# Optimization experiments

Measured on AMD Instinct MI355X. Metric: run time of the kernel, lower is better.

## Reference

```python
import jax, jax.numpy as jnp
import numpy as np

DIM = 64          # out_channels == mamba d_model
D_INNER = 2 * DIM # mamba expand=2
D_STATE = 16
DT_RANK = 4       # ceil(DIM/16)
D_CONV = 4


def setup_inputs() -> dict:
    key = jax.random.key(0)
    ks = jax.random.split(key, 12)
    B, Cin, H, W = 4, 32, 192, 192
    x = jax.random.normal(ks[0], (B, Cin, H, W), jnp.float32)
    conv_w = jax.random.normal(ks[1], (DIM, Cin, 4, 4), jnp.float32) * (1.0 / np.sqrt(Cin * 16))
    conv_b = jnp.zeros((DIM,), jnp.float32)
    ln_g = jnp.ones((DIM,), jnp.float32)
    ln_b = jnp.zeros((DIM,), jnp.float32)
    in_proj_w = jax.random.normal(ks[2], (2 * D_INNER, DIM), jnp.float32) * (1.0 / np.sqrt(DIM))
    conv1d_w = jax.random.normal(ks[3], (D_INNER, 1, D_CONV), jnp.float32) * (1.0 / np.sqrt(D_CONV))
    conv1d_b = jnp.zeros((D_INNER,), jnp.float32)
    x_proj_w = jax.random.normal(ks[4], (DT_RANK + 2 * D_STATE, D_INNER), jnp.float32) * (1.0 / np.sqrt(D_INNER))
    dt_proj_w = jax.random.normal(ks[5], (D_INNER, DT_RANK), jnp.float32) * (DT_RANK ** -0.5)
    dt_proj_b = jnp.log(jnp.expm1(jnp.exp(jax.random.uniform(ks[6], (D_INNER,), jnp.float32,
                jnp.log(1e-3), jnp.log(1e-1)))))  # softplus-inverse of dt in [1e-3,1e-1]
    A_log = jnp.log(jnp.tile(jnp.arange(1, D_STATE + 1, dtype=jnp.float32)[None, :], (D_INNER, 1)))
    D = jnp.ones((D_INNER,), jnp.float32)
    out_proj_w = jax.random.normal(ks[7], (DIM, D_INNER), jnp.float32) * (1.0 / np.sqrt(D_INNER))
    return {"x": x, "conv_w": conv_w, "conv_b": conv_b, "ln_g": ln_g, "ln_b": ln_b,
            "in_proj_w": in_proj_w, "conv1d_w": conv1d_w, "conv1d_b": conv1d_b,
            "x_proj_w": x_proj_w, "dt_proj_w": dt_proj_w, "dt_proj_b": dt_proj_b,
            "A_log": A_log, "D": D, "out_proj_w": out_proj_w}


def _mamba(seq, in_proj_w, conv1d_w, conv1d_b, x_proj_w, dt_proj_w, dt_proj_b, A_log, D, out_proj_w):
    # seq: (B, L, DIM)
    Bb, L, _ = seq.shape
    xz = seq @ in_proj_w.T                          # (B, L, 2*d_inner)
    xm, z = jnp.split(xz, 2, axis=-1)
    # causal depthwise conv1d along L
    xc = jnp.transpose(xm, (0, 2, 1))               # (B, d_inner, L)
    xc = jnp.pad(xc, ((0, 0), (0, 0), (D_CONV - 1, 0)))
    xc = jax.lax.conv_general_dilated(xc, conv1d_w, (1,), 'VALID',
                                      dimension_numbers=('NCH', 'OIH', 'NCH'),
                                      feature_group_count=D_INNER)
    xm = jax.nn.silu(jnp.transpose(xc + conv1d_b[None, :, None], (0, 2, 1)))  # (B, L, d_inner)
    x_dbl = xm @ x_proj_w.T                         # (B, L, dt_rank + 2*d_state)
    dt, Bs, Cs = jnp.split(x_dbl, [DT_RANK, DT_RANK + D_STATE], axis=-1)
    dt = jax.nn.softplus(dt @ dt_proj_w.T + dt_proj_b)  # (B, L, d_inner)
    A = -jnp.exp(A_log)                             # (d_inner, d_state)
    dA = jnp.exp(dt[..., None] * A)                 # (B, L, d_inner, d_state)
    dBx = (dt * xm)[..., None] * Bs[:, :, None, :]  # (B, L, d_inner, d_state)

    def step(h, t):
        dA_t, dBx_t, C_t = t
        h = dA_t * h + dBx_t                        # (B, d_inner, d_state)
        return h, jnp.einsum('bds,bs->bd', h, C_t)

    h0 = jnp.zeros((Bb, D_INNER, D_STATE), seq.dtype)
    _, ys = jax.lax.scan(step, h0, (jnp.swapaxes(dA, 0, 1), jnp.swapaxes(dBx, 0, 1), jnp.swapaxes(Cs, 0, 1)))
    y = jnp.swapaxes(ys, 0, 1) + xm * D             # (B, L, d_inner)
    y = y * jax.nn.silu(z)
    return y @ out_proj_w.T                          # (B, L, DIM)


def reference(x, conv_w, conv_b, ln_g, ln_b, in_proj_w, conv1d_w, conv1d_b,
              x_proj_w, dt_proj_w, dt_proj_b, A_log, D, out_proj_w):
    # ReflectionPad2d(1) + Conv2d(k=4, s=2)
    xp = jnp.pad(x, ((0, 0), (0, 0), (1, 1), (1, 1)), mode='reflect')
    xc = jax.lax.conv_general_dilated(xp, conv_w, (2, 2), 'VALID',
                                      dimension_numbers=('NCHW', 'OIHW', 'NCHW'))
    xc = xc + conv_b[None, :, None, None]           # (B, DIM, H/2, W/2)
    Bb, C, H, W = xc.shape
    seq = jnp.transpose(xc.reshape(Bb, C, H * W), (0, 2, 1))  # (B, L, C)
    mu = seq.mean(-1, keepdims=True)
    var = seq.var(-1, keepdims=True)
    nrm = (seq - mu) * jax.lax.rsqrt(var + 1e-5) * ln_g + ln_b
    out = _mamba(nrm, in_proj_w, conv1d_w, conv1d_b, x_proj_w, dt_proj_w,
                 dt_proj_b, A_log, D, out_proj_w) + seq        # SingleMambaBlock residual
    out = jnp.transpose(out, (0, 2, 1)).reshape(Bb, C, H, W)
    return out + xc                                 # outer residual in Mamba_block.forward
```

## Files before the change

### kernel.cpp

```cpp
#include <hip/hip_runtime.h>
#include <hip/hip_bf16.h>

#define B_   4
#define CIN  32
#define HIN  192
#define WIN  192
#define HO   96
#define WO   96
#define L_   9216
#define C_   64
#define DI   128
#define DS   16
#define NC   256
#define CL   36

typedef unsigned short u16t;
typedef unsigned int   u32t;
typedef short s16x8 __attribute__((ext_vector_type(8)));
typedef float f32x4 __attribute__((ext_vector_type(4)));

__device__ __forceinline__ u16t f2b(float f) {
    u32t u = __float_as_uint(f);
    return (u16t)((u + 0x7fffu + ((u >> 16) & 1u)) >> 16);
}
__device__ __forceinline__ float b2f(u16t h) { return __uint_as_float(((u32t)h) << 16); }
__device__ __forceinline__ void split2(float v, u16t& hi, u16t& lo) {
    hi = f2b(v);
    lo = f2b(v - b2f(hi));
}

#define MFMA16(a, b, c) __builtin_amdgcn_mfma_f32_16x16x32_bf16((a), (b), (c), 0, 0, 0)

__global__ __launch_bounds__(256) void k0_prep(
    const float* __restrict__ ipw, const float* __restrict__ xpw,
    const float* __restrict__ dtw, const float* __restrict__ opw,
    const float* __restrict__ cw,
    u16t* __restrict__ W2p, u16t* __restrict__ Wcp, u16t* __restrict__ W6p,
    u16t* __restrict__ Bp)
{
    int i = blockIdx.x * 256 + threadIdx.x;
    if (i < 32768) {
        int e = i & 7, ln = (i >> 3) & 63, hl = (i >> 9) & 1;
        int nt = (i >> 10) & 15, kt = i >> 14;
        int n = nt * 16 + (ln & 15), k = kt * 32 + (ln >> 4) * 8 + e;
        u16t hi, lo; split2(ipw[n * 64 + k], hi, lo);
        W2p[i] = hl ? lo : hi;
    } else if (i < 32768 + 40960) {
        int j = i - 32768;
        int e = j & 7, ln = (j >> 3) & 63, hl = (j >> 9) & 1;
        int r = j >> 10; int nt = r % 10, kt = r / 10;
        int n = nt * 16 + (ln & 15), k = kt * 32 + (ln >> 4) * 8 + e;
        float v;
        if (n < 128) {
            v = dtw[n * 4 + 0] * xpw[0 * 128 + k] + dtw[n * 4 + 1] * xpw[1 * 128 + k]
              + dtw[n * 4 + 2] * xpw[2 * 128 + k] + dtw[n * 4 + 3] * xpw[3 * 128 + k];
        } else if (n < 144) {
            v = xpw[(4 + n - 128) * 128 + k];
        } else {
            v = xpw[(20 + n - 144) * 128 + k];
        }
        u16t hi, lo; split2(v, hi, lo);
        Wcp[j] = hl ? lo : hi;
    } else if (i < 32768 + 40960 + 16384) {
        int j = i - 32768 - 40960;
        int e = j & 7, ln = (j >> 3) & 63, hl = (j >> 9) & 1;
        int nt = (j >> 10) & 3, kt = j >> 12;
        int n = nt * 16 + (ln & 15), k = kt * 32 + (ln >> 4) * 8 + e;
        u16t hi, lo; split2(opw[n * 128 + k], hi, lo);
        W6p[j] = hl ? lo : hi;
    } else if (i < 32768 + 40960 + 16384 + 32768) {
        int j = i - 32768 - 40960 - 16384;
        int e = j & 7, ln = (j >> 3) & 63, nt = (j >> 9) & 3, kt = j >> 11;
        int n = nt * 16 + (ln & 15), k = kt * 32 + (ln >> 4) * 8 + e;
        Bp[j] = f2b(cw[n * 512 + k]);
    }
}

__global__ __launch_bounds__(256) void k1_conv_ln(
    const float* __restrict__ x, const u16t* __restrict__ Bp,
    const float* __restrict__ cb, const float* __restrict__ g,
    const float* __restrict__ be,
    float* __restrict__ seq, float* __restrict__ nrm)
{
    __shared__ u16t At[64 * 136];
    const int t = threadIdx.x;
    const int pix0 = blockIdx.x * 64;
    const int b = pix0 / L_;
    const int l0 = pix0 % L_;
    const int wave = t >> 6, ln = t & 63;
    const int quad = ln >> 4, col = ln & 15;

    const int kk = t & 127;
    const int m0 = t >> 7;
    const int kh = (kk >> 2) & 3, kw = kk & 3, cil = kk >> 4;

    f32x4 acc[4];
    #pragma unroll
    for (int nt = 0; nt < 4; ++nt) acc[nt] = (f32x4){0.f, 0.f, 0.f, 0.f};

    const u16t* arow = &At[(wave * 16 + col) * 136 + quad * 8];

    for (int cc = 0; cc < 4; ++cc) {
        __syncthreads();
        const float* xb = x + (b * CIN + cc * 8 + cil) * (HIN * WIN);
        #pragma unroll 4
        for (int j = 0; j < 32; ++j) {
            int m = m0 + 2 * j;
            int l = l0 + m;
            int oh = l / WO, ow = l - oh * WO;
            int ih = 2 * oh + kh - 1; ih = ih < 0 ? 1 : (ih >= HIN ? 2 * HIN - 2 - ih : ih);
            int iw = 2 * ow + kw - 1; iw = iw < 0 ? 1 : (iw >= WIN ? 2 * WIN - 2 - iw : iw);
            At[m * 136 + kk] = f2b(xb[ih * WIN + iw]);
        }
        __syncthreads();

        #pragma unroll
        for (int ktl = 0; ktl < 4; ++ktl) {
            s16x8 a = *reinterpret_cast<const s16x8*>(arow + ktl * 32);
            const u16t* bpb = Bp + (cc * 4 + ktl) * 2048 + ln * 8;
            #pragma unroll
            for (int nt = 0; nt < 4; ++nt) {
                s16x8 bf = *reinterpret_cast<const s16x8*>(bpb + nt * 512);
                acc[nt] = MFMA16(a, bf, acc[nt]);
            }
        }
    }

    float gv[4], bv[4], cbv[4];
    #pragma unroll
    for (int nt = 0; nt < 4; ++nt) {
        gv[nt] = g[nt * 16 + col];
        bv[nt] = be[nt * 16 + col];
        cbv[nt] = cb[nt * 16 + col];
    }
    #pragma unroll
    for (int r = 0; r < 4; ++r) {
        float v0 = acc[0][r] + cbv[0];
        float v1 = acc[1][r] + cbv[1];
        float v2 = acc[2][r] + cbv[2];
        float v3 = acc[3][r] + cbv[3];
        float s1 = (v0 + v1) + (v2 + v3);
        float s2 = (v0 * v0 + v1 * v1) + (v2 * v2 + v3 * v3);
        #pragma unroll
        for (int mk = 1; mk <= 8; mk <<= 1) {
            s1 += __shfl_xor(s1, mk);
            s2 += __shfl_xor(s2, mk);
        }
        float mu = s1 * (1.0f / 64.0f);
        float var = s2 * (1.0f / 64.0f) - mu * mu;
        float rs = rsqrtf(var + 1e-5f);
        int pix = pix0 + wave * 16 + quad * 4 + r;
        float* sp = seq + pix * 64 + col;
        float* np = nrm + pix * 64 + col;
        sp[0]  = v0; sp[16] = v1; sp[32] = v2; sp[48] = v3;
        np[0]  = (v0 - mu) * rs * gv[0] + bv[0];
        np[16] = (v1 - mu) * rs * gv[1] + bv[1];
        np[32] = (v2 - mu) * rs * gv[2] + bv[2];
        np[48] = (v3 - mu) * rs * gv[3] + bv[3];
    }
}

__global__ __launch_bounds__(256) void g2_inproj(
    const float* __restrict__ nrm, const u16t* __restrict__ W2p,
    float* __restrict__ xm, float* __restrict__ sz)
{
    __shared__ u16t Ah[64 * 72], Al[64 * 72];
    const int t = threadIdx.x;
    const int row0 = blockIdx.x * 64;

    for (int idx = t; idx < 1024; idx += 256) {
        int r = idx >> 4, kq = (idx & 15) * 4;
        float4 v = *reinterpret_cast<const float4*>(nrm + (row0 + r) * 64 + kq);
        u16t h, l;
        split2(v.x, h, l); Ah[r * 72 + kq + 0] = h; Al[r * 72 + kq + 0] = l;
        split2(v.y, h, l); Ah[r * 72 + kq + 1] = h; Al[r * 72 + kq + 1] = l;
        split2(v.z, h, l); Ah[r * 72 + kq + 2] = h; Al[r * 72 + kq + 2] = l;
        split2(v.w, h, l); Ah[r * 72 + kq + 3] = h; Al[r * 72 + kq + 3] = l;
    }
    __syncthreads();

    const int wave = t >> 6, ln = t & 63, quad = ln >> 4, col = ln & 15;
    f32x4 acc[16];
    #pragma unroll
    for (int nt = 0; nt < 16; ++nt) acc[nt] = (f32x4){0.f, 0.f, 0.f, 0.f};

    const int abase = (wave * 16 + col) * 72 + quad * 8;
    #pragma unroll
    for (int kt = 0; kt < 2; ++kt) {
        s16x8 ah = *reinterpret_cast<const s16x8*>(Ah + abase + kt * 32);
        s16x8 al = *reinterpret_cast<const s16x8*>(Al + abase + kt * 32);
        const u16t* bb = W2p + (kt * 16) * 1024 + ln * 8;
        #pragma unroll
        for (int nt = 0; nt < 16; ++nt) {
            s16x8 bh = *reinterpret_cast<const s16x8*>(bb + nt * 1024);
            s16x8 bl = *reinterpret_cast<const s16x8*>(bb + nt * 1024 + 512);
            acc[nt] = MFMA16(al, bh, acc[nt]);
            acc[nt] = MFMA16(ah, bl, acc[nt]);
            acc[nt] = MFMA16(ah, bh, acc[nt]);
        }
    }

    const int mrow = row0 + wave * 16 + quad * 4;
    #pragma unroll
    for (int nt = 0; nt < 16; ++nt) {
        int n = nt * 16 + col;
        #pragma unroll
        for (int r = 0; r < 4; ++r) {
            float v = acc[nt][r];
            if (n < 128) {
                xm[(mrow + r) * DI + n] = v;
            } else {
                sz[(mrow + r) * DI + (n - 128)] = v / (1.f + __expf(-v));
            }
        }
    }
}

__global__ __launch_bounds__(256) void k3_dwconv(
    const float* __restrict__ xm, const float* __restrict__ w,
    const float* __restrict__ bia, float* __restrict__ u)
{
    const int gid = blockIdx.x * 256 + threadIdx.x;
    const int c = gid & 127;
    const int g = gid >> 7;
    const int bl0 = g * 4;
    const int l0 = bl0 % L_;

    float w0 = w[c * 4 + 0], w1 = w[c * 4 + 1];
    float w2 = w[c * 4 + 2], w3 = w[c * 4 + 3];
    float bv = bia[c];

    float xv[7];
    if (l0 == 0) { xv[0] = xv[1] = xv[2] = 0.f; }
    else {
        xv[0] = xm[(bl0 - 3) * DI + c];
        xv[1] = xm[(bl0 - 2) * DI + c];
        xv[2] = xm[(bl0 - 1) * DI + c];
    }
    #pragma unroll
    for (int j = 0; j < 4; ++j) xv[3 + j] = xm[(bl0 + j) * DI + c];

    #pragma unroll
    for (int j = 0; j < 4; ++j) {
        float a = bv + xv[j] * w0 + xv[j + 1] * w1 + xv[j + 2] * w2 + xv[j + 3] * w3;
        u[(bl0 + j) * DI + c] = a / (1.f + __expf(-a));
    }
}

__global__ __launch_bounds__(256) void g4_xproj(
    const float* __restrict__ u, const u16t* __restrict__ Wcp,
    const float* __restrict__ dtb,
    float* __restrict__ dt, float* __restrict__ Bs, float* __restrict__ Cs)
{
    __shared__ u16t Ah[64 * 136], Al[64 * 136];
    const int t = threadIdx.x;
    const int row0 = blockIdx.x * 64;

    for (int idx = t; idx < 2048; idx += 256) {
        int r = idx >> 5, kq = (idx & 31) * 4;
        float4 v = *reinterpret_cast<const float4*>(u + (row0 + r) * DI + kq);
        u16t h, l;
        split2(v.x, h, l); Ah[r * 136 + kq + 0] = h; Al[r * 136 + kq + 0] = l;
        split2(v.y, h, l); Ah[r * 136 + kq + 1] = h; Al[r * 136 + kq + 1] = l;
        split2(v.z, h, l); Ah[r * 136 + kq + 2] = h; Al[r * 136 + kq + 2] = l;
        split2(v.w, h, l); Ah[r * 136 + kq + 3] = h; Al[r * 136 + kq + 3] = l;
    }
    __syncthreads();

    const int wave = t >> 6, ln = t & 63, quad = ln >> 4, col = ln & 15;
    f32x4 acc[10];
    #pragma unroll
    for (int nt = 0; nt < 10; ++nt) acc[nt] = (f32x4){0.f, 0.f, 0.f, 0.f};

    const int abase = (wave * 16 + col) * 136 + quad * 8;
    #pragma unroll
    for (int kt = 0; kt < 4; ++kt) {
        s16x8 ah = *reinterpret_cast<const s16x8*>(Ah + abase + kt * 32);
        s16x8 al = *reinterpret_cast<const s16x8*>(Al + abase + kt * 32);
        const u16t* bb = Wcp + (kt * 10) * 1024 + ln * 8;
        #pragma unroll
        for (int nt = 0; nt < 10; ++nt) {
            s16x8 bh = *reinterpret_cast<const s16x8*>(bb + nt * 1024);
            s16x8 bl = *reinterpret_cast<const s16x8*>(bb + nt * 1024 + 512);
            acc[nt] = MFMA16(al, bh, acc[nt]);
            acc[nt] = MFMA16(ah, bl, acc[nt]);
            acc[nt] = MFMA16(ah, bh, acc[nt]);
        }
    }

    const int mrow = row0 + wave * 16 + quad * 4;
    #pragma unroll
    for (int nt = 0; nt < 8; ++nt) {
        int n = nt * 16 + col;
        float db = dtb[n];
        #pragma unroll
        for (int r = 0; r < 4; ++r) {
            float v = acc[nt][r] + db;
            v = v > 20.f ? v : log1pf(__expf(v));
            dt[(mrow + r) * DI + n] = v;
        }
    }
    #pragma unroll
    for (int r = 0; r < 4; ++r) {
        Bs[(mrow + r) * DS + col] = acc[8][r];
        Cs[(mrow + r) * DS + col] = acc[9][r];
    }
}

__global__ __launch_bounds__(128) void k5a(
    const float* __restrict__ dt, const float* __restrict__ u,
    const float* __restrict__ Bsb, const float* __restrict__ alog,
    float* __restrict__ P, float* __restrict__ HP)
{
    const int bk = blockIdx.x;
    const int b = bk / NC, k = bk - b * NC;
    const int c = threadIdx.x;
    float As[DS];
    #pragma unroll
    for (int s = 0; s < DS; ++s) As[s] = -__expf(alog[c * DS + s]);
    float Pp[DS], hp[DS];
    #pragma unroll
    for (int s = 0; s < DS; ++s) { Pp[s] = 1.f; hp[s] = 0.f; }

    const int l0 = k * CL;
    for (int i = 0; i < CL; ++i) {
        const int row = b * L_ + l0 + i;
        float dtv = dt[row * DI + c];
        float uv = u[row * DI + c];
        float dtu = dtv * uv;
        const float4* Bq = reinterpret_cast<const float4*>(Bsb + row * DS);
        float Bv[DS];
        #pragma unroll
        for (int q = 0; q < 4; ++q)
            *reinterpret_cast<float4*>(&Bv[q * 4]) = Bq[q];
        #pragma unroll
        for (int s = 0; s < DS; ++s) {
            float dA = __expf(dtv * As[s]);
            hp[s] = dA * hp[s] + dtu * Bv[s];
            Pp[s] *= dA;
        }
    }
    float* Pd = P + bk * 2048 + c * DS;
    float* Hd = HP + bk * 2048 + c * DS;
    #pragma unroll
    for (int q = 0; q < 4; ++q) {
        reinterpret_cast<float4*>(Pd)[q] = *reinterpret_cast<float4*>(&Pp[q * 4]);
        reinterpret_cast<float4*>(Hd)[q] = *reinterpret_cast<float4*>(&hp[q * 4]);
    }
}

__global__ __launch_bounds__(256) void k5b(
    float* __restrict__ P, const float* __restrict__ HP)
{
    const int t = blockIdx.x * 256 + threadIdx.x;
    const int b = t >> 11, cs = t & 2047;
    float carry = 0.f;
    for (int k = 0; k < NC; ++k) {
        const int idx = (b * NC + k) * 2048 + cs;
        float p = P[idx];
        float hp = HP[idx];
        P[idx] = carry;
        carry = hp + p * carry;
    }
}

__global__ __launch_bounds__(128) void k5c(
    const float* __restrict__ dt, float* __restrict__ u,
    const float* __restrict__ Bsb, const float* __restrict__ Csb,
    const float* __restrict__ sz, const float* __restrict__ alog,
    const float* __restrict__ Db, const float* __restrict__ HI)
{
    const int bk = blockIdx.x;
    const int b = bk / NC, k = bk - b * NC;
    const int c = threadIdx.x;
    float As[DS];
    #pragma unroll
    for (int s = 0; s < DS; ++s) As[s] = -__expf(alog[c * DS + s]);
    const float Dc = Db[c];
    float h[DS];
    const float* Hs = HI + bk * 2048 + c * DS;
    #pragma unroll
    for (int q = 0; q < 4; ++q)
        *reinterpret_cast<float4*>(&h[q * 4]) = reinterpret_cast<const float4*>(Hs)[q];

    const int l0 = k * CL;
    for (int i = 0; i < CL; ++i) {
        const int row = b * L_ + l0 + i;
        float dtv = dt[row * DI + c];
        float uv = u[row * DI + c];
        float szv = sz[row * DI + c];
        float dtu = dtv * uv;
        const float4* Bq = reinterpret_cast<const float4*>(Bsb + row * DS);
        const float4* Cq = reinterpret_cast<const float4*>(Csb + row * DS);
        float Bv[DS], Cv[DS];
        #pragma unroll
        for (int q = 0; q < 4; ++q) {
            *reinterpret_cast<float4*>(&Bv[q * 4]) = Bq[q];
            *reinterpret_cast<float4*>(&Cv[q * 4]) = Cq[q];
        }
        float ya[4] = {0.f, 0.f, 0.f, 0.f};
        #pragma unroll
        for (int s = 0; s < DS; ++s) {
            float dA = __expf(dtv * As[s]);
            h[s] = dA * h[s] + dtu * Bv[s];
            ya[s & 3] += h[s] * Cv[s];
        }
        float yv = (ya[0] + ya[1]) + (ya[2] + ya[3]);
        u[row * DI + c] = (yv + uv * Dc) * szv;
    }
}

__global__ __launch_bounds__(256) void g6_outproj(
    const float* __restrict__ yc, const u16t* __restrict__ W6p,
    const float* __restrict__ seq, float* __restrict__ out)
{
    __shared__ u16t smem[2 * 64 * 136];
    u16t* Ah = smem;
    u16t* Al = smem + 64 * 136;
    const int t = threadIdx.x;
    const int row0 = blockIdx.x * 64;

    for (int idx = t; idx < 2048; idx += 256) {
        int r = idx >> 5, kq = (idx & 31) * 4;
        float4 v = *reinterpret_cast<const float4*>(yc + (row0 + r) * DI + kq);
        u16t h, l;
        split2(v.x, h, l); Ah[r * 136 + kq + 0] = h; Al[r * 136 + kq + 0] = l;
        split2(v.y, h, l); Ah[r * 136 + kq + 1] = h; Al[r * 136 + kq + 1] = l;
        split2(v.z, h, l); Ah[r * 136 + kq + 2] = h; Al[r * 136 + kq + 2] = l;
        split2(v.w, h, l); Ah[r * 136 + kq + 3] = h; Al[r * 136 + kq + 3] = l;
    }
    __syncthreads();

    const int wave = t >> 6, ln = t & 63, quad = ln >> 4, col = ln & 15;
    f32x4 acc[4];
    #pragma unroll
    for (int nt = 0; nt < 4; ++nt) acc[nt] = (f32x4){0.f, 0.f, 0.f, 0.f};

    const int abase = (wave * 16 + col) * 136 + quad * 8;
    #pragma unroll
    for (int kt = 0; kt < 4; ++kt) {
        s16x8 ah = *reinterpret_cast<const s16x8*>(Ah + abase + kt * 32);
        s16x8 al = *reinterpret_cast<const s16x8*>(Al + abase + kt * 32);
        const u16t* bb = W6p + (kt * 4) * 1024 + ln * 8;
        #pragma unroll
        for (int nt = 0; nt < 4; ++nt) {
            s16x8 bh = *reinterpret_cast<const s16x8*>(bb + nt * 1024);
            s16x8 bl = *reinterpret_cast<const s16x8*>(bb + nt * 1024 + 512);
            acc[nt] = MFMA16(al, bh, acc[nt]);
            acc[nt] = MFMA16(ah, bl, acc[nt]);
            acc[nt] = MFMA16(ah, bh, acc[nt]);
        }
    }
    __syncthreads();

    float* yT = reinterpret_cast<float*>(smem);
    const int ml = wave * 16 + quad * 4;
    #pragma unroll
    for (int nt = 0; nt < 4; ++nt) {
        int n = nt * 16 + col;
        #pragma unroll
        for (int r = 0; r < 4; ++r) {
            int row = row0 + ml + r;
            yT[n * 68 + ml + r] = acc[nt][r] + 2.f * seq[row * 64 + n];
        }
    }
    __syncthreads();

    const int n = t >> 2;
    const int lq = (t & 3) * 16;
    const int b = row0 / L_;
    const int l0 = row0 % L_;
    float* op = out + (b * 64 + n) * L_ + l0 + lq;
    #pragma unroll
    for (int q = 0; q < 4; ++q) {
        float4 v = *reinterpret_cast<float4*>(&yT[n * 68 + lq + q * 4]);
        *reinterpret_cast<float4*>(op + q * 4) = v;
    }
}

extern "C" void kernel_launch(void* const* d_in, const int* in_sizes, int n_in,
                              void* d_out, int out_size, void* d_ws, size_t ws_size,
                              hipStream_t stream)
{
    const float* x    = (const float*)d_in[0];
    const float* cw   = (const float*)d_in[1];
    const float* cb   = (const float*)d_in[2];
    const float* g    = (const float*)d_in[3];
    const float* be   = (const float*)d_in[4];
    const float* ipw  = (const float*)d_in[5];
    const float* c1w  = (const float*)d_in[6];
    const float* c1b  = (const float*)d_in[7];
    const float* xpw  = (const float*)d_in[8];
    const float* dtw  = (const float*)d_in[9];
    const float* dtb  = (const float*)d_in[10];
    const float* alog = (const float*)d_in[11];
    const float* Db   = (const float*)d_in[12];
    const float* opw  = (const float*)d_in[13];

    float* ws  = (float*)d_ws;
    float* seq = ws;
    float* nrm = seq + 2359296;
    float* xm  = nrm + 2359296;
    float* sz  = xm + 4718592;
    float* u   = sz + 4718592;
    float* dt  = u + 4718592;
    u16t*  W2p = (u16t*)(dt + 4718592);
    u16t*  Wcp = W2p + 32768;
    u16t*  W6p = Wcp + 40960;
    u16t*  Bp  = W6p + 16384;
    float* Bs  = nrm;
    float* Cs  = nrm + 589824;
    float* P   = xm;
    float* HP  = xm + 2097152;

    k0_prep   <<<480, 256, 0, stream>>>(ipw, xpw, dtw, opw, cw, W2p, Wcp, W6p, Bp);
    k1_conv_ln<<<576, 256, 0, stream>>>(x, Bp, cb, g, be, seq, nrm);
    g2_inproj <<<576, 256, 0, stream>>>(nrm, W2p, xm, sz);
    k3_dwconv <<<4608, 256, 0, stream>>>(xm, c1w, c1b, u);
    g4_xproj  <<<576, 256, 0, stream>>>(u, Wcp, dtb, dt, Bs, Cs);
    k5a       <<<B_ * NC, 128, 0, stream>>>(dt, u, Bs, alog, P, HP);
    k5b       <<<32, 256, 0, stream>>>(P, HP);
    k5c       <<<B_ * NC, 128, 0, stream>>>(dt, u, Bs, Cs, sz, alog, Db, P);
    g6_outproj<<<576, 256, 0, stream>>>(u, W6p, seq, (float*)d_out);
}
```

Baseline: 261.5 us.

## Fuse depthwise conv into in_proj and out_proj into scan output kernel

The causal depthwise conv1d is folded into the in_proj GEMM kernel: each block keeps its xm tile in shared memory and recomputes the 3-row halo with a scalar FP32 dot product against a transposed weight copy, so the xm round trip through global memory and the separate conv launch go away. The out_proj GEMM, both residual adds and the transposed output store move into the final scan kernel, which writes its y chunk (36 rows) to shared memory as split bf16 instead of to global memory. In exchange, every in_proj block pays the redundant halo work, and the out_proj MFMA runs on partially empty 16-row tiles with a scalar, poorly coalesced output store.

After: 279.4 us. +6.8%, slower.

```diff
diff --git a/kernel.cpp b/kernel.cpp
--- a/kernel.cpp
+++ b/kernel.cpp
@@ -36,7 +36,7 @@
     const float* __restrict__ dtw, const float* __restrict__ opw,
     const float* __restrict__ cw,
     u16t* __restrict__ W2p, u16t* __restrict__ Wcp, u16t* __restrict__ W6p,
-    u16t* __restrict__ Bp)
+    u16t* __restrict__ Bp, float* __restrict__ W2t)
 {
     int i = blockIdx.x * 256 + threadIdx.x;
     if (i < 32768) {
@@ -73,6 +73,10 @@
         int e = j & 7, ln = (j >> 3) & 63, nt = (j >> 9) & 3, kt = j >> 11;
         int n = nt * 16 + (ln & 15), k = kt * 32 + (ln >> 4) * 8 + e;
         Bp[j] = f2b(cw[n * 512 + k]);
+    } else if (i < 32768 + 40960 + 16384 + 32768 + 16384) {
+        int j = i - 32768 - 40960 - 16384 - 32768;
+        int k = j >> 8, n = j & 255;
+        W2t[j] = ipw[n * 64 + k];
     }
 }
 
@@ -160,13 +164,17 @@
     }
 }
 
-__global__ __launch_bounds__(256) void g2_inproj(
+__global__ __launch_bounds__(256) void g2_inproj_conv(
     const float* __restrict__ nrm, const u16t* __restrict__ W2p,
-    float* __restrict__ xm, float* __restrict__ sz)
+    const float* __restrict__ W2t, const float* __restrict__ c1w,
+    const float* __restrict__ c1b,
+    float* __restrict__ u, float* __restrict__ sz)
 {
     __shared__ u16t Ah[64 * 72], Al[64 * 72];
+    __shared__ float xmL[67 * 132];
     const int t = threadIdx.x;
     const int row0 = blockIdx.x * 64;
+    const int l0 = row0 % L_;
 
     for (int idx = t; idx < 1024; idx += 256) {
         int r = idx >> 4, kq = (idx & 15) * 4;
@@ -177,6 +185,16 @@
         split2(v.z, h, l); Ah[r * 72 + kq + 2] = h; Al[r * 72 + kq + 2] = l;
         split2(v.w, h, l); Ah[r * 72 + kq + 3] = h; Al[r * 72 + kq + 3] = l;
     }
+    for (int idx = t; idx < 384; idx += 256) {
+        int j = idx >> 7, n = idx & 127;
+        float acc = 0.f;
+        if (l0 != 0) {
+            const float* nr = nrm + (row0 - 3 + j) * 64;
+            #pragma unroll 4
+            for (int k = 0; k < 64; ++k) acc += nr[k] * W2t[k * 256 + n];
+        }
+        xmL[j * 132 + n] = acc;
+    }
     __syncthreads();
 
     const int wave = t >> 6, ln = t & 63, quad = ln >> 4, col = ln & 15;
@@ -200,7 +218,7 @@
         }
     }
 
-    const int mrow = row0 + wave * 16 + quad * 4;
+    const int ml = wave * 16 + quad * 4;
     #pragma unroll
     for (int nt = 0; nt < 16; ++nt) {
         int n = nt * 16 + col;
@@ -208,42 +226,25 @@
         for (int r = 0; r < 4; ++r) {
             float v = acc[nt][r];
             if (n < 128) {
-                xm[(mrow + r) * DI + n] = v;
+                xmL[(3 + ml + r) * 132 + n] = v;
             } else {
-                sz[(mrow + r) * DI + (n - 128)] = v / (1.f + __expf(-v));
+                sz[(row0 + ml + r) * DI + (n - 128)] = v / (1.f + __expf(-v));
             }
         }
     }
-}
-
-__global__ __launch_bounds__(256) void k3_dwconv(
-    const float* __restrict__ xm, const float* __restrict__ w,
-    const float* __restrict__ bia, float* __restrict__ u)
-{
-    const int gid = blockIdx.x * 256 + threadIdx.x;
-    const int c = gid & 127;
-    const int g = gid >> 7;
-    const int bl0 = g * 4;
-    const int l0 = bl0 % L_;
-
-    float w0 = w[c * 4 + 0], w1 = w[c * 4 + 1];
-    float w2 = w[c * 4 + 2], w3 = w[c * 4 + 3];
-    float bv = bia[c];
-
-    float xv[7];
-    if (l0 == 0) { xv[0] = xv[1] = xv[2] = 0.f; }
-    else {
-        xv[0] = xm[(bl0 - 3) * DI + c];
-        xv[1] = xm[(bl0 - 2) * DI + c];
-        xv[2] = xm[(bl0 - 1) * DI + c];
-    }
-    #pragma unroll
-    for (int j = 0; j < 4; ++j) xv[3 + j] = xm[(bl0 + j) * DI + c];
-
-    #pragma unroll
-    for (int j = 0; j < 4; ++j) {
-        float a = bv + xv[j] * w0 + xv[j + 1] * w1 + xv[j + 2] * w2 + xv[j + 3] * w3;
-        u[(bl0 + j) * DI + c] = a / (1.f + __expf(-a));
+    __syncthreads();
+
+    const int n = t & 127;
+    const float w0 = c1w[n * 4 + 0], w1 = c1w[n * 4 + 1];
+    const float w2 = c1w[n * 4 + 2], w3 = c1w[n * 4 + 3];
+    const float bv = c1b[n];
+    const int rb = t >> 7;
+    #pragma unroll 4
+    for (int i = 0; i < 32; ++i) {
+        int r = rb + 2 * i;
+        float a = bv + xmL[(r + 0) * 132 + n] * w0 + xmL[(r + 1) * 132 + n] * w1
+                     + xmL[(r + 2) * 132 + n] * w2 + xmL[(r + 3) * 132 + n] * w3;
+        u[(row0 + r) * DI + n] = a / (1.f + __expf(-a));
     }
 }
 
@@ -364,12 +365,15 @@
     }
 }
 
-__global__ __launch_bounds__(128) void k5c(
-    const float* __restrict__ dt, float* __restrict__ u,
+__global__ __launch_bounds__(128) void k5c_out(
+    const float* __restrict__ dt, const float* __restrict__ u,
     const float* __restrict__ Bsb, const float* __restrict__ Csb,
     const float* __restrict__ sz, const float* __restrict__ alog,
-    const float* __restrict__ Db, const float* __restrict__ HI)
-{
+    const float* __restrict__ Db, const float* __restrict__ HI,
+    const float* __restrict__ seq, const u16t* __restrict__ W6p,
+    float* __restrict__ out)
+{
+    __shared__ u16t Yh[64 * 136], Yl[64 * 136];
     const int bk = blockIdx.x;
     const int b = bk / NC, k = bk - b * NC;
     const int c = threadIdx.x;
@@ -405,76 +409,66 @@
             h[s] = dA * h[s] + dtu * Bv[s];
             ya[s & 3] += h[s] * Cv[s];
         }
-        float yv = (ya[0] + ya[1]) + (ya[2] + ya[3]);
-        u[row * DI + c] = (yv + uv * Dc) * szv;
-    }
-}
-
-__global__ __launch_bounds__(256) void g6_outproj(
-    const float* __restrict__ yc, const u16t* __restrict__ W6p,
-    const float* __restrict__ seq, float* __restrict__ out)
-{
-    __shared__ u16t smem[2 * 64 * 136];
-    u16t* Ah = smem;
-    u16t* Al = smem + 64 * 136;
-    const int t = threadIdx.x;
-    const int row0 = blockIdx.x * 64;
-
-    for (int idx = t; idx < 2048; idx += 256) {
-        int r = idx >> 5, kq = (idx & 31) * 4;
-        float4 v = *reinterpret_cast<const float4*>(yc + (row0 + r) * DI + kq);
-        u16t h, l;
-        split2(v.x, h, l); Ah[r * 136 + kq + 0] = h; Al[r * 136 + kq + 0] = l;
-        split2(v.y, h, l); Ah[r * 136 + kq + 1] = h; Al[r * 136 + kq + 1] = l;
-        split2(v.z, h, l); Ah[r * 136 + kq + 2] = h; Al[r * 136 + kq + 2] = l;
-        split2(v.w, h, l); Ah[r * 136 + kq + 3] = h; Al[r * 136 + kq + 3] = l;
+        float yv = ((ya[0] + ya[1]) + (ya[2] + ya[3]) + uv * Dc) * szv;
+        u16t hi, lo; split2(yv, hi, lo);
+        Yh[i * 136 + c] = hi;
+        Yl[i * 136 + c] = lo;
     }
     __syncthreads();
 
-    const int wave = t >> 6, ln = t & 63, quad = ln >> 4, col = ln & 15;
-    f32x4 acc[4];
-    #pragma unroll
-    for (int nt = 0; nt < 4; ++nt) acc[nt] = (f32x4){0.f, 0.f, 0.f, 0.f};
-
-    const int abase = (wave * 16 + col) * 136 + quad * 8;
-    #pragma unroll
-    for (int kt = 0; kt < 4; ++kt) {
-        s16x8 ah = *reinterpret_cast<const s16x8*>(Ah + abase + kt * 32);
-        s16x8 al = *reinterpret_cast<const s16x8*>(Al + abase + kt * 32);
-        const u16t* bb = W6p + (kt * 4) * 1024 + ln * 8;
+    const int wave = c >> 6, ln = c & 63, quad = ln >> 4, col = ln & 15;
+    f32x4 acc[2][4];
+    #pragma unroll
+    for (int mt = 0; mt < 2; ++mt)
+        #pragma unroll
+        for (int nt = 0; nt < 4; ++nt) acc[mt][nt] = (f32x4){0.f, 0.f, 0.f, 0.f};
+
+    #pragma unroll
+    for (int mt = 0; mt < 2; ++mt) {
+        const int m = (wave * 2 + mt) * 16 + col;
+        if (m >= 48 && wave == 1 && mt == 1) {}
+        const int abase = m * 136 + quad * 8;
+        #pragma unroll
+        for (int kt = 0; kt < 4; ++kt) {
+            s16x8 ah = (m < CL + 16) ? *reinterpret_cast<const s16x8*>(Yh + abase + kt * 32)
+                                     : (s16x8){0,0,0,0,0,0,0,0};
+            s16x8 al = (m < CL + 16) ? *reinterpret_cast<const s16x8*>(Yl + abase + kt * 32)
+                                     : (s16x8){0,0,0,0,0,0,0,0};
+            const u16t* bb = W6p + (kt * 4) * 1024 + ln * 8;
+            #pragma unroll
+            for (int nt = 0; nt < 4; ++nt) {
+                s16x8 bh = *reinterpret_cast<const s16x8*>(bb + nt * 1024);
+                s16x8 bl = *reinterpret_cast<const s16x8*>(bb + nt * 1024 + 512);
+                acc[mt][nt] = MFMA16(al, bh, acc[mt][nt]);
+                acc[mt][nt] = MFMA16(ah, bl, acc[mt][nt]);
+                acc[mt][nt] = MFMA16(ah, bh, acc[mt][nt]);
+            }
+        }
+    }
+    __syncthreads();
+
+    float* oT = reinterpret_cast<float*>(Yh);
+    #pragma unroll
+    for (int mt = 0; mt < 2; ++mt) {
+        const int mb = (wave * 2 + mt) * 16 + quad * 4;
         #pragma unroll
         for (int nt = 0; nt < 4; ++nt) {
-            s16x8 bh = *reinterpret_cast<const s16x8*>(bb + nt * 1024);
-            s16x8 bl = *reinterpret_cast<const s16x8*>(bb + nt * 1024 + 512);
-            acc[nt] = MFMA16(al, bh, acc[nt]);
-            acc[nt] = MFMA16(ah, bl, acc[nt]);
-            acc[nt] = MFMA16(ah, bh, acc[nt]);
+            const int n = nt * 16 + col;
+            #pragma unroll
+            for (int r = 0; r < 4; ++r) {
+                const int m = mb + r;
+                if (m < CL)
+                    oT[n * 37 + m] = acc[mt][nt][r]
+                                   + 2.f * seq[(b * L_ + l0 + m) * 64 + n];
+            }
         }
     }
     __syncthreads();
 
-    float* yT = reinterpret_cast<float*>(smem);
-    const int ml = wave * 16 + quad * 4;
-    #pragma unroll
-    for (int nt = 0; nt < 4; ++nt) {
-        int n = nt * 16 + col;
-        #pragma unroll
-        for (int r = 0; r < 4; ++r) {
-            int row = row0 + ml + r;
-            yT[n * 68 + ml + r] = acc[nt][r] + 2.f * seq[row * 64 + n];
-        }
-    }
-    __syncthreads();
-
-    const int n = t >> 2;
-    const int lq = (t & 3) * 16;
-    const int b = row0 / L_;
-    const int l0 = row0 % L_;
-    float* op = out + (b * 64 + n) * L_ + l0 + lq;
-    #pragma unroll
-    for (int q = 0; q < 4; ++q) {
-        float4 v = *reinterpret_cast<float4*>(&yT[n * 68 + lq + q * 4]);
-        *reinterpret_cast<float4*>(op + q * 4) = v;
+    for (int i = 0; i < 18; ++i) {
+        int idx = i * 128 + c;
+        int n = idx / CL, l = idx - n * CL;
+        out[(b * 64 + n) * L_ + l0 + l] = oT[n * 37 + l];
     }
 }
 
@@ -500,26 +494,25 @@
     float* ws  = (float*)d_ws;
     float* seq = ws;
     float* nrm = seq + 2359296;
-    float* xm  = nrm + 2359296;
-    float* sz  = xm + 4718592;
-    float* u   = sz + 4718592;
-    float* dt  = u + 4718592;
-    u16t*  W2p = (u16t*)(dt + 4718592);
+    float* u   = nrm + 2359296;
+    float* sz  = u + 4718592;
+    float* dt  = sz + 4718592;
+    float* P   = dt + 4718592;
+    float* HP  = P + 2097152;
+    u16t*  W2p = (u16t*)(HP + 2097152);
     u16t*  Wcp = W2p + 32768;
     u16t*  W6p = Wcp + 40960;
     u16t*  Bp  = W6p + 16384;
+    float* W2t = (float*)(Bp + 32768);
     float* Bs  = nrm;
     float* Cs  = nrm + 589824;
-    float* P   = xm;
-    float* HP  = xm + 2097152;
-
-    k0_prep   <<<480, 256, 0, stream>>>(ipw, xpw, dtw, opw, cw, W2p, Wcp, W6p, Bp);
-    k1_conv_ln<<<576, 256, 0, stream>>>(x, Bp, cb, g, be, seq, nrm);
-    g2_inproj <<<576, 256, 0, stream>>>(nrm, W2p, xm, sz);
-    k3_dwconv <<<4608, 256, 0, stream>>>(xm, c1w, c1b, u);
-    g4_xproj  <<<576, 256, 0, stream>>>(u, Wcp, dtb, dt, Bs, Cs);
-    k5a       <<<B_ * NC, 128, 0, stream>>>(dt, u, Bs, alog, P, HP);
-    k5b       <<<32, 256, 0, stream>>>(P, HP);
-    k5c       <<<B_ * NC, 128, 0, stream>>>(dt, u, Bs, Cs, sz, alog, Db, P);
-    g6_outproj<<<576, 256, 0, stream>>>(u, W6p, seq, (float*)d_out);
-}
+
+    k0_prep       <<<544, 256, 0, stream>>>(ipw, xpw, dtw, opw, cw, W2p, Wcp, W6p, Bp, W2t);
+    k1_conv_ln    <<<576, 256, 0, stream>>>(x, Bp, cb, g, be, seq, nrm);
+    g2_inproj_conv<<<576, 256, 0, stream>>>(nrm, W2p, W2t, c1w, c1b, u, sz);
+    g4_xproj      <<<576, 256, 0, stream>>>(u, Wcp, dtb, dt, Bs, Cs);
+    k5a           <<<B_ * NC, 128, 0, stream>>>(dt, u, Bs, alog, P, HP);
+    k5b           <<<32, 256, 0, stream>>>(P, HP);
+    k5c_out       <<<B_ * NC, 128, 0, stream>>>(dt, u, Bs, Cs, sz, alog, Db, P,
+                                                seq, W6p, (float*)d_out);
+}
```

## Fuse selective-scan output pass with out_proj MFMA GEMM and residual store

Applied to the files above, without the earlier changes.

Merges the second scan pass with the output projection. Each chunk's gated y values are split into bf16 hi/lo pairs in shared memory and multiplied against W6 with MFMA in the same block. This removes the round trip of writing y to global memory and reading it back, and drops a separate kernel launch. The cost is padded MFMA tiles, since only 36 of 64 rows are valid, and output stores that cover just 36 contiguous elements per channel. The prefix-combine kernel also moves to 64-thread blocks, spreading its serial chains over more CUs.

New measurement: 260.2 us. No clear change (-0.5%).

```diff
diff --git a/kernel.cpp b/kernel.cpp
--- a/kernel.cpp
+++ b/kernel.cpp
@@ -349,10 +349,10 @@
     }
 }
 
-__global__ __launch_bounds__(256) void k5b(
+__global__ __launch_bounds__(64) void k5b(
     float* __restrict__ P, const float* __restrict__ HP)
 {
-    const int t = blockIdx.x * 256 + threadIdx.x;
+    const int t = blockIdx.x * 64 + threadIdx.x;
     const int b = t >> 11, cs = t & 2047;
     float carry = 0.f;
     for (int k = 0; k < NC; ++k) {
@@ -364,12 +364,15 @@
     }
 }
 
-__global__ __launch_bounds__(128) void k5c(
-    const float* __restrict__ dt, float* __restrict__ u,
+__global__ __launch_bounds__(128) void k5c_out(
+    const float* __restrict__ dt, const float* __restrict__ u,
     const float* __restrict__ Bsb, const float* __restrict__ Csb,
     const float* __restrict__ sz, const float* __restrict__ alog,
-    const float* __restrict__ Db, const float* __restrict__ HI)
-{
+    const float* __restrict__ Db, const float* __restrict__ HI,
+    const float* __restrict__ seq, const u16t* __restrict__ W6p,
+    float* __restrict__ out)
+{
+    __shared__ u16t Yh[64 * 136], Yl[64 * 136];
     const int bk = blockIdx.x;
     const int b = bk / NC, k = bk - b * NC;
     const int c = threadIdx.x;
@@ -405,76 +408,65 @@
             h[s] = dA * h[s] + dtu * Bv[s];
             ya[s & 3] += h[s] * Cv[s];
         }
-        float yv = (ya[0] + ya[1]) + (ya[2] + ya[3]);
-        u[row * DI + c] = (yv + uv * Dc) * szv;
-    }
-}
-
-__global__ __launch_bounds__(256) void g6_outproj(
-    const float* __restrict__ yc, const u16t* __restrict__ W6p,
-    const float* __restrict__ seq, float* __restrict__ out)
-{
-    __shared__ u16t smem[2 * 64 * 136];
-    u16t* Ah = smem;
-    u16t* Al = smem + 64 * 136;
-    const int t = threadIdx.x;
-    const int row0 = blockIdx.x * 64;
-
-    for (int idx = t; idx < 2048; idx += 256) {
-        int r = idx >> 5, kq = (idx & 31) * 4;
-        float4 v = *reinterpret_cast<const float4*>(yc + (row0 + r) * DI + kq);
-        u16t h, l;
-        split2(v.x, h, l); Ah[r * 136 + kq + 0] = h; Al[r * 136 + kq + 0] = l;
-        split2(v.y, h, l); Ah[r * 136 + kq + 1] = h; Al[r * 136 + kq + 1] = l;
-        split2(v.z, h, l); Ah[r * 136 + kq + 2] = h; Al[r * 136 + kq + 2] = l;
-        split2(v.w, h, l); Ah[r * 136 + kq + 3] = h; Al[r * 136 + kq + 3] = l;
+        float yv = ((ya[0] + ya[1]) + (ya[2] + ya[3]) + uv * Dc) * szv;
+        u16t hi, lo; split2(yv, hi, lo);
+        Yh[i * 136 + c] = hi;
+        Yl[i * 136 + c] = lo;
     }
     __syncthreads();
 
-    const int wave = t >> 6, ln = t & 63, quad = ln >> 4, col = ln & 15;
-    f32x4 acc[4];
-    #pragma unroll
-    for (int nt = 0; nt < 4; ++nt) acc[nt] = (f32x4){0.f, 0.f, 0.f, 0.f};
-
-    const int abase = (wave * 16 + col) * 136 + quad * 8;
-    #pragma unroll
-    for (int kt = 0; kt < 4; ++kt) {
-        s16x8 ah = *reinterpret_cast<const s16x8*>(Ah + abase + kt * 32);
-        s16x8 al = *reinterpret_cast<const s16x8*>(Al + abase + kt * 32);
-        const u16t* bb = W6p + (kt * 4) * 1024 + ln * 8;
+    const int wave = c >> 6, ln = c & 63, quad = ln >> 4, col = ln & 15;
+    f32x4 acc[2][4];
+    #pragma unroll
+    for (int mt = 0; mt < 2; ++mt)
+        #pragma unroll
+        for (int nt = 0; nt < 4; ++nt) acc[mt][nt] = (f32x4){0.f, 0.f, 0.f, 0.f};
+
+    #pragma unroll
+    for (int mt = 0; mt < 2; ++mt) {
+        const int m = (wave * 2 + mt) * 16 + col;
+        const int abase = m * 136 + quad * 8;
+        #pragma unroll
+        for (int kt = 0; kt < 4; ++kt) {
+            s16x8 ah = (m < CL + 16) ? *reinterpret_cast<const s16x8*>(Yh + abase + kt * 32)
+                                     : (s16x8){0,0,0,0,0,0,0,0};
+            s16x8 al = (m < CL + 16) ? *reinterpret_cast<const s16x8*>(Yl + abase + kt * 32)
+                                     : (s16x8){0,0,0,0,0,0,0,0};
+            const u16t* bb = W6p + (kt * 4) * 1024 + ln * 8;
+            #pragma unroll
+            for (int nt = 0; nt < 4; ++nt) {
+                s16x8 bh = *reinterpret_cast<const s16x8*>(bb + nt * 1024);
+                s16x8 bl = *reinterpret_cast<const s16x8*>(bb + nt * 1024 + 512);
+                acc[mt][nt] = MFMA16(al, bh, acc[mt][nt]);
+                acc[mt][nt] = MFMA16(ah, bl, acc[mt][nt]);
+                acc[mt][nt] = MFMA16(ah, bh, acc[mt][nt]);
+            }
+        }
+    }
+    __syncthreads();
+
+    float* oT = reinterpret_cast<float*>(Yh);
+    #pragma unroll
+    for (int mt = 0; mt < 2; ++mt) {
+        const int mb = (wave * 2 + mt) * 16 + quad * 4;
         #pragma unroll
         for (int nt = 0; nt < 4; ++nt) {
-            s16x8 bh = *reinterpret_cast<const s16x8*>(bb + nt * 1024);
-            s16x8 bl = *reinterpret_cast<const s16x8*>(bb + nt * 1024 + 512);
-            acc[nt] = MFMA16(al, bh, acc[nt]);
-            acc[nt] = MFMA16(ah, bl, acc[nt]);
-            acc[nt] = MFMA16(ah, bh, acc[nt]);
+            const int n = nt * 16 + col;
+            #pragma unroll
+            for (int r = 0; r < 4; ++r) {
+                const int m = mb + r;
+                if (m < CL)
+                    oT[n * 37 + m] = acc[mt][nt][r]
+                                   + 2.f * seq[(b * L_ + l0 + m) * 64 + n];
+            }
         }
     }
     __syncthreads();
 
-    float* yT = reinterpret_cast<float*>(smem);
-    const int ml = wave * 16 + quad * 4;
-    #pragma unroll
-    for (int nt = 0; nt < 4; ++nt) {
-        int n = nt * 16 + col;
-        #pragma unroll
-        for (int r = 0; r < 4; ++r) {
-            int row = row0 + ml + r;
-            yT[n * 68 + ml + r] = acc[nt][r] + 2.f * seq[row * 64 + n];
-        }
-    }
-    __syncthreads();
-
-    const int n = t >> 2;
-    const int lq = (t & 3) * 16;
-    const int b = row0 / L_;
-    const int l0 = row0 % L_;
-    float* op = out + (b * 64 + n) * L_ + l0 + lq;
-    #pragma unroll
-    for (int q = 0; q < 4; ++q) {
-        float4 v = *reinterpret_cast<float4*>(&yT[n * 68 + lq + q * 4]);
-        *reinterpret_cast<float4*>(op + q * 4) = v;
+    for (int i = 0; i < 18; ++i) {
+        int idx = i * 128 + c;
+        int n = idx / CL, l = idx - n * CL;
+        out[(b * 64 + n) * L_ + l0 + l] = oT[n * 37 + l];
     }
 }
 
@@ -519,7 +511,7 @@
     k3_dwconv <<<4608, 256, 0, stream>>>(xm, c1w, c1b, u);
     g4_xproj  <<<576, 256, 0, stream>>>(u, Wcp, dtb, dt, Bs, Cs);
     k5a       <<<B_ * NC, 128, 0, stream>>>(dt, u, Bs, alog, P, HP);
-    k5b       <<<32, 256, 0, stream>>>(P, HP);
-    k5c       <<<B_ * NC, 128, 0, stream>>>(dt, u, Bs, Cs, sz, alog, Db, P);
-    g6_outproj<<<576, 256, 0, stream>>>(u, W6p, seq, (float*)d_out);
-}
+    k5b      <<<128, 64, 0, stream>>>(P, HP);
+    k5c_out   <<<B_ * NC, 128, 0, stream>>>(dt, u, Bs, Cs, sz, alog, Db, P,
+                                            seq, W6p, (float*)d_out);
+}
```
